# Optimization experiments

Measured on AMD Instinct MI355X. Metric: run time of the kernel, lower is better.

## Reference

```python
import jax, jax.numpy as jnp
import numpy as np

B, D, P, C = 4096, 512, 256, 8
LAMBDA = 1.0


def setup_inputs() -> dict:
    key = jax.random.key(0)
    k1, k2, k3, k4 = jax.random.split(key, 4)
    x = jax.random.normal(k1, (B, D), dtype=jnp.float32)
    y = jax.random.randint(k2, (B,), 0, C, dtype=jnp.int32)
    prototypes = jax.random.normal(k3, (P, D), dtype=jnp.float32)
    # omega initialized as eye + 0.01*randn per class, like the torch module
    omega = jnp.eye(D, dtype=jnp.float32)[None] + 0.01 * jax.random.normal(k4, (C, D, D), dtype=jnp.float32)
    prototype_labels = (jnp.arange(P, dtype=jnp.int32) % C).astype(jnp.int32)
    return {"x": x, "y": y, "prototypes": prototypes, "omega": omega, "prototype_labels": prototype_labels}


def reference(x, y, prototypes, omega, prototype_labels):
    # transformed inputs per class: tx[c,b,:] = omega[c] @ x[b]
    tx = jnp.einsum('cij,bj->cbi', omega, x)                     # [C,B,D]
    # transformed prototypes under every class omega, then pick each
    # prototype's own class matrix: tp[p,:] = omega[label[p]] @ w[p]
    tp_all = jnp.einsum('cij,pj->cpi', omega, prototypes)        # [C,P,D]
    tp = tp_all[prototype_labels, jnp.arange(P)]                 # [P,D]
    # squared distances via expansion ||a-b||^2 = |a|^2 + |b|^2 - 2ab
    dots = jnp.einsum('cbd,pd->cbp', tx, tp)                     # [C,B,P]
    x2 = jnp.sum(tx * tx, axis=-1)                               # [C,B]
    p2 = jnp.sum(tp * tp, axis=-1)                               # [P]
    dist_all = x2[:, :, None] + p2[None, None, :] - 2.0 * dots   # [C,B,P]
    # each prototype uses the omega of its own class
    dist = dist_all[prototype_labels, :, jnp.arange(P)].T        # [B,P]
    same = prototype_labels[None, :] == y[:, None]               # [B,P]
    inf = jnp.float32(jnp.inf)
    pos = jnp.min(jnp.where(same, dist, inf), axis=1)            # [B]
    neg = jnp.min(jnp.where(same, inf, dist), axis=1)            # [B]
    mu = (pos - neg) / (pos + neg)
    loss = jnp.mean(jax.nn.sigmoid(LAMBDA * mu))
    loss = loss + 0.01 * jnp.linalg.norm(omega.reshape(-1))
    return loss
```

## Files before the change

### kernel.cpp

```cpp
#include <hip/hip_runtime.h>
#include <math.h>

typedef unsigned short ushort_t;
typedef __attribute__((ext_vector_type(8))) short short8;
typedef __attribute__((ext_vector_type(4))) float f32x4;

#define B_N 4096
#define D_N 512
#define P_N 256
#define C_N 8

#define ACC_OFF   0
#define P2G_OFF   256
#define X2_OFF    1280
#define XB_OFF    132352
#define OMB_OFF   (XB_OFF + B_N*D_N*2)
#define TPG_OFF   (OMB_OFF + C_N*D_N*D_N*2)
#define UG_OFF    (TPG_OFF + P_N*D_N*2)
#define OMBT_OFF  (UG_OFF + P_N*D_N*2)
#define MINB_OFF  OMBT_OFF

#define MFMA16(a, b, c) __builtin_amdgcn_mfma_f32_16x16x32_bf16(a, b, c, 0, 0, 0)

__device__ inline ushort_t f2bf(float f) {
    union { float f; unsigned u; } v; v.f = f;
    unsigned r = v.u + 0x7FFFu + ((v.u >> 16) & 1u);
    return (ushort_t)(r >> 16);
}

__device__ __forceinline__ void gll16(const ushort_t* g, ushort_t* l) {
    __builtin_amdgcn_global_load_lds((const __attribute__((address_space(1))) void*)g,
                                     (__attribute__((address_space(3))) void*)l, 16, 0, 0);
}

__global__ void k_cast(const float* __restrict__ x, const float* __restrict__ omega,
                       ushort_t* __restrict__ xb, ushort_t* __restrict__ omb,
                       ushort_t* __restrict__ ombT, float* __restrict__ oss) {
    __shared__ ushort_t T[64][72];
    __shared__ float red[4];
    int t = threadIdx.x;
    if (blockIdx.x < 1024) {
        int idx = blockIdx.x * 256 + t;
        const float4* x4 = (const float4*)x;
        float4 a = x4[idx * 2], b = x4[idx * 2 + 1];
        union { ushort_t s[8]; uint4 v; } o;
        o.s[0] = f2bf(a.x); o.s[1] = f2bf(a.y); o.s[2] = f2bf(a.z); o.s[3] = f2bf(a.w);
        o.s[4] = f2bf(b.x); o.s[5] = f2bf(b.y); o.s[6] = f2bf(b.z); o.s[7] = f2bf(b.w);
        ((uint4*)xb)[idx] = o.v;
        return;
    }
    int bid = blockIdx.x - 1024;
    int c = bid >> 6, by = (bid >> 3) & 7, bx = bid & 7;
    int r0 = by * 64, c0 = bx * 64;
    int r = t >> 2, seg = t & 3;
    const float* src = omega + ((size_t)c * D_N + r0 + r) * D_N + c0 + seg * 16;
    float4 v0 = ((const float4*)src)[0], v1 = ((const float4*)src)[1];
    float4 v2 = ((const float4*)src)[2], v3 = ((const float4*)src)[3];
    float s = v0.x*v0.x + v0.y*v0.y + v0.z*v0.z + v0.w*v0.w
            + v1.x*v1.x + v1.y*v1.y + v1.z*v1.z + v1.w*v1.w
            + v2.x*v2.x + v2.y*v2.y + v2.z*v2.z + v2.w*v2.w
            + v3.x*v3.x + v3.y*v3.y + v3.z*v3.z + v3.w*v3.w;
    union { ushort_t s[16]; uint4 v[2]; } o;
    float vv[16] = {v0.x,v0.y,v0.z,v0.w, v1.x,v1.y,v1.z,v1.w,
                    v2.x,v2.y,v2.z,v2.w, v3.x,v3.y,v3.z,v3.w};
    #pragma unroll
    for (int j = 0; j < 16; ++j) o.s[j] = f2bf(vv[j]);
    uint4* dst = (uint4*)(omb + ((size_t)c * D_N + r0 + r) * D_N + c0 + seg * 16);
    dst[0] = o.v[0]; dst[1] = o.v[1];
    #pragma unroll
    for (int j = 0; j < 16; ++j) T[seg * 16 + j][r] = o.s[j];
    __syncthreads();
    int jr = t >> 2, sg2 = t & 3;
    uint4 w0 = *(uint4*)&T[jr][sg2 * 16];
    uint4 w1 = *(uint4*)&T[jr][sg2 * 16 + 8];
    uint4* dstT = (uint4*)(ombT + ((size_t)c * D_N + c0 + jr) * D_N + r0 + sg2 * 16);
    dstT[0] = w0; dstT[1] = w1;
    #pragma unroll
    for (int off = 32; off > 0; off >>= 1) s += __shfl_down(s, off);
    if ((t & 63) == 0) red[t >> 6] = s;
    __syncthreads();
    if (t == 0) atomicAdd(oss, red[0] + red[1] + red[2] + red[3]);
}

__global__ __launch_bounds__(256) void k_tp(const float* __restrict__ prot,
                                            const ushort_t* __restrict__ omb,
                                            ushort_t* __restrict__ tpg,
                                            float* __restrict__ p2g) {
    int i0 = blockIdx.x * 64, c = blockIdx.y;
    __shared__ ushort_t As[32][72];
    __shared__ ushort_t Bs[64][72];
    int t = threadIdx.x, w = t >> 6, lane = t & 63;
    int g = lane >> 4, cl = lane & 15;
    f32x4 acc[2] = {{0,0,0,0},{0,0,0,0}};
    for (int k0 = 0; k0 < D_N; k0 += 64) {
        __syncthreads();
        {
            int m = t >> 3, seg = t & 7;
            const float* ap = prot + ((size_t)(c + 8 * m)) * D_N + k0 + seg * 8;
            float4 u0 = ((const float4*)ap)[0], u1 = ((const float4*)ap)[1];
            union { ushort_t s[8]; uint4 v; } o;
            o.s[0]=f2bf(u0.x); o.s[1]=f2bf(u0.y); o.s[2]=f2bf(u0.z); o.s[3]=f2bf(u0.w);
            o.s[4]=f2bf(u1.x); o.s[5]=f2bf(u1.y); o.s[6]=f2bf(u1.z); o.s[7]=f2bf(u1.w);
            *(uint4*)&As[m][seg * 8] = o.v;
        }
        {
            int r = t >> 2, sg = t & 3;
            const uint4* bp = (const uint4*)(omb + ((size_t)c * D_N + i0 + r) * D_N + k0 + sg * 16);
            *(uint4*)&Bs[r][sg * 16] = bp[0];
            *(uint4*)&Bs[r][sg * 16 + 8] = bp[1];
        }
        __syncthreads();
        #pragma unroll
        for (int kk = 0; kk < 2; ++kk) {
            int koff = kk * 32 + g * 8;
            short8 bfr = *(const short8*)&Bs[w * 16 + cl][koff];
            #pragma unroll
            for (int mt = 0; mt < 2; ++mt) {
                short8 afr = *(const short8*)&As[mt * 16 + cl][koff];
                acc[mt] = MFMA16(afr, bfr, acc[mt]);
            }
        }
    }
    #pragma unroll
    for (int mt = 0; mt < 2; ++mt)
        #pragma unroll
        for (int reg = 0; reg < 4; ++reg) {
            float v = acc[mt][reg];
            int m = mt * 16 + g * 4 + reg;
            int i = i0 + w * 16 + cl;
            tpg[((size_t)c * 32 + m) * D_N + i] = f2bf(v);
            float s = v * v;
            s += __shfl_xor(s, 1); s += __shfl_xor(s, 2);
            s += __shfl_xor(s, 4); s += __shfl_xor(s, 8);
            if (cl == 0) atomicAdd(&p2g[c * 32 + m], s);
        }
}

__global__ __launch_bounds__(256) void k_u(const ushort_t* __restrict__ tpg,
                                           const ushort_t* __restrict__ ombT,
                                           ushort_t* __restrict__ ug) {
    int j0 = blockIdx.x * 64, c = blockIdx.y;
    __shared__ ushort_t As[32][72];
    __shared__ ushort_t Bs[64][72];
    int t = threadIdx.x, w = t >> 6, lane = t & 63;
    int g = lane >> 4, cl = lane & 15;
    f32x4 acc[2] = {{0,0,0,0},{0,0,0,0}};
    for (int k0 = 0; k0 < D_N; k0 += 64) {
        __syncthreads();
        {
            int m = t >> 3, seg = t & 7;
            *(uint4*)&As[m][seg * 8] =
                *(const uint4*)(tpg + ((size_t)c * 32 + m) * D_N + k0 + seg * 8);
        }
        {
            int r = t >> 2, sg = t & 3;
            const uint4* bp = (const uint4*)(ombT + ((size_t)c * D_N + j0 + r) * D_N + k0 + sg * 16);
            *(uint4*)&Bs[r][sg * 16] = bp[0];
            *(uint4*)&Bs[r][sg * 16 + 8] = bp[1];
        }
        __syncthreads();
        #pragma unroll
        for (int kk = 0; kk < 2; ++kk) {
            int koff = kk * 32 + g * 8;
            short8 bfr = *(const short8*)&Bs[w * 16 + cl][koff];
            #pragma unroll
            for (int mt = 0; mt < 2; ++mt) {
                short8 afr = *(const short8*)&As[mt * 16 + cl][koff];
                acc[mt] = MFMA16(afr, bfr, acc[mt]);
            }
        }
    }
    #pragma unroll
    for (int mt = 0; mt < 2; ++mt)
        #pragma unroll
        for (int reg = 0; reg < 4; ++reg) {
            int m = mt * 16 + g * 4 + reg;
            int j = j0 + w * 16 + cl;
            ug[((size_t)c * 32 + m) * D_N + j] = f2bf(acc[mt][reg]);
        }
}

__global__ __launch_bounds__(256, 2) void k_x2d(const ushort_t* __restrict__ xb,
                                                const ushort_t* __restrict__ omb,
                                                const ushort_t* __restrict__ ug,
                                                const float* __restrict__ p2g,
                                                float* __restrict__ x2,
                                                float* __restrict__ minb) {
    int c  = blockIdx.y;
    int b0 = blockIdx.z * 128;
    int t = threadIdx.x, w = t >> 6, lane = t & 63;
    int g = lane >> 4, cl = lane & 15;
    int srow = lane >> 2, spos = lane & 3;
    int ch = ((g - (cl >> 1)) & 3) * 8;

    __shared__ ushort_t Xs[2][128][32];
    __shared__ ushort_t Os[2][256][32];
    __shared__ float red[128][2];

    if (blockIdx.x < 2) {
        int i0 = blockIdx.x * 256;
        int qr = w >> 1, qc = w & 1;
        f32x4 acc[4][8];
        #pragma unroll
        for (int mt = 0; mt < 4; ++mt)
            #pragma unroll
            for (int nt = 0; nt < 8; ++nt) acc[mt][nt] = (f32x4){0,0,0,0};
        #pragma unroll
        for (int i = 0; i < 2; ++i) {
            int rb = w * 32 + i * 16;
            int r  = rb + srow;
            int cg = (spos + (r >> 1)) & 3;
            gll16(xb + (size_t)(b0 + r) * D_N + cg * 8, &Xs[0][rb][0]);
        }
        #pragma unroll
        for (int i = 0; i < 4; ++i) {
            int rb = w * 64 + i * 16;
            int r  = rb + srow;
            int cg = (spos + (r >> 1)) & 3;
            gll16(omb + ((size_t)c * D_N + i0 + r) * D_N + cg * 8, &Os[0][rb][0]);
        }
        __syncthreads();
        for (int s = 0; s < 16; ++s) {
            int cb = s & 1, nb = cb ^ 1;
            if (s < 15) {
                int k1 = (s + 1) * 32;
                #pragma unroll
                for (int i = 0; i < 2; ++i) {
                    int rb = w * 32 + i * 16;
                    int r  = rb + srow;
                    int cg = (spos + (r >> 1)) & 3;
                    gll16(xb + (size_t)(b0 + r) * D_N + k1 + cg * 8, &Xs[nb][rb][0]);
                }
                #pragma unroll
                for (int i = 0; i < 4; ++i) {
                    int rb = w * 64 + i * 16;
                    int r  = rb + srow;
                    int cg = (spos + (r >> 1)) & 3;
                    gll16(omb + ((size_t)c * D_N + i0 + r) * D_N + k1 + cg * 8, &Os[nb][rb][0]);
                }
            }
            short8 a[4], b[8];
            #pragma unroll
            for (int mt = 0; mt < 4; ++mt)
                a[mt] = *(const short8*)&Xs[cb][qr * 64 + mt * 16 + cl][ch];
            #pragma unroll
            for (int nt = 0; nt < 8; ++nt)
                b[nt] = *(const short8*)&Os[cb][qc * 128 + nt * 16 + cl][ch];
            #pragma unroll
            for (int mt = 0; mt < 4; ++mt)
                #pragma unroll
                for (int nt = 0; nt < 8; ++nt)
                    acc[mt][nt] = MFMA16(a[mt], b[nt], acc[mt][nt]);
            __syncthreads();
        }
        #pragma unroll
        for (int mt = 0; mt < 4; ++mt)
            #pragma unroll
            for (int reg = 0; reg < 4; ++reg) {
                float s = 0.f;
                #pragma unroll
                for (int nt = 0; nt < 8; ++nt) s += acc[mt][nt][reg] * acc[mt][nt][reg];
                s += __shfl_xor(s, 1); s += __shfl_xor(s, 2);
                s += __shfl_xor(s, 4); s += __shfl_xor(s, 8);
                if (cl == 0) red[qr * 64 + mt * 16 + g * 4 + reg][qc] = s;
            }
        __syncthreads();
        if (t < 128) atomicAdd(&x2[(size_t)(b0 + t) * C_N + c], red[t][0] + red[t][1]);
    } else {
        f32x4 acc[2][2];
        #pragma unroll
        for (int mt = 0; mt < 2; ++mt)
            #pragma unroll
            for (int nt = 0; nt < 2; ++nt) acc[mt][nt] = (f32x4){0,0,0,0};
        #pragma unroll
        for (int i = 0; i < 2; ++i) {
            int rb = w * 32 + i * 16;
            int r  = rb + srow;
            int cg = (spos + (r >> 1)) & 3;
            gll16(xb + (size_t)(b0 + r) * D_N + cg * 8, &Xs[0][rb][0]);
        }
        if (w < 2) {
            int rb = w * 16;
            int r  = rb + srow;
            int cg = (spos + (r >> 1)) & 3;
            gll16(ug + ((size_t)c * 32 + r) * D_N + cg * 8, &Os[0][rb][0]);
        }
        __syncthreads();
        for (int s = 0; s < 16; ++s) {
            int cb = s & 1, nb = cb ^ 1;
            if (s < 15) {
                int k1 = (s + 1) * 32;
                #pragma unroll
                for (int i = 0; i < 2; ++i) {
                    int rb = w * 32 + i * 16;
                    int r  = rb + srow;
                    int cg = (spos + (r >> 1)) & 3;
                    gll16(xb + (size_t)(b0 + r) * D_N + k1 + cg * 8, &Xs[nb][rb][0]);
                }
                if (w < 2) {
                    int rb = w * 16;
                    int r  = rb + srow;
                    int cg = (spos + (r >> 1)) & 3;
                    gll16(ug + ((size_t)c * 32 + r) * D_N + k1 + cg * 8, &Os[nb][rb][0]);
                }
            }
            short8 a[2], b[2];
            #pragma unroll
            for (int mt = 0; mt < 2; ++mt)
                a[mt] = *(const short8*)&Xs[cb][w * 32 + mt * 16 + cl][ch];
            #pragma unroll
            for (int nt = 0; nt < 2; ++nt)
                b[nt] = *(const short8*)&Os[cb][nt * 16 + cl][ch];
            #pragma unroll
            for (int mt = 0; mt < 2; ++mt)
                #pragma unroll
                for (int nt = 0; nt < 2; ++nt)
                    acc[mt][nt] = MFMA16(a[mt], b[nt], acc[mt][nt]);
            __syncthreads();
        }
        #pragma unroll
        for (int mt = 0; mt < 2; ++mt)
            #pragma unroll
            for (int reg = 0; reg < 4; ++reg) {
                float v = INFINITY;
                #pragma unroll
                for (int nt = 0; nt < 2; ++nt) {
                    int q = c * 32 + nt * 16 + cl;
                    v = fminf(v, p2g[q] - 2.f * acc[mt][nt][reg]);
                }
                v = fminf(v, __shfl_xor(v, 1)); v = fminf(v, __shfl_xor(v, 2));
                v = fminf(v, __shfl_xor(v, 4)); v = fminf(v, __shfl_xor(v, 8));
                if (cl == 0)
                    minb[(size_t)(b0 + w * 32 + mt * 16 + g * 4 + reg) * C_N + c] = v;
            }
    }
}

__global__ void k_mu(const float* __restrict__ x2, const float* __restrict__ minb,
                     const int* __restrict__ y, float* __restrict__ accs,
                     float* __restrict__ out) {
    int t = threadIdx.x;
    int b = blockIdx.x * 256 + t;
    int yb = y[b];
    float d[8];
    #pragma unroll
    for (int cc = 0; cc < 8; ++cc)
        d[cc] = x2[(size_t)b * C_N + cc] + minb[(size_t)b * C_N + cc];
    float pos = d[yb];
    float neg = INFINITY;
    #pragma unroll
    for (int cc = 0; cc < 8; ++cc)
        if (cc != yb) neg = fminf(neg, d[cc]);
    float mu = (pos - neg) / (pos + neg);
    float s = 1.f / (1.f + expf(-mu));
    #pragma unroll
    for (int off = 32; off > 0; off >>= 1) s += __shfl_down(s, off);
    __shared__ float red[4];
    if ((t & 63) == 0) red[t >> 6] = s;
    __syncthreads();
    if (t == 0) {
        atomicAdd(accs, red[0] + red[1] + red[2] + red[3]);
        __threadfence();
        unsigned n = atomicAdd((unsigned int*)(accs + 2), 1u);
        if (n == (unsigned)(B_N / 256 - 1)) {
            float ls  = atomicAdd(accs, 0.f);
            float oss = atomicAdd(accs + 1, 0.f);
            out[0] = ls * (1.f / (float)B_N) + 0.01f * sqrtf(oss);
        }
    }
}

extern "C" void kernel_launch(void* const* d_in, const int* in_sizes, int n_in,
                              void* d_out, int out_size, void* d_ws, size_t ws_size,
                              hipStream_t stream) {
    (void)in_sizes; (void)n_in; (void)out_size; (void)ws_size;
    const float* x     = (const float*)d_in[0];
    const int*   y     = (const int*)d_in[1];
    const float* prot  = (const float*)d_in[2];
    const float* omega = (const float*)d_in[3];

    char* ws = (char*)d_ws;
    float*    accs = (float*)(ws + ACC_OFF);
    float*    p2g  = (float*)(ws + P2G_OFF);
    float*    x2   = (float*)(ws + X2_OFF);
    ushort_t* xb   = (ushort_t*)(ws + XB_OFF);
    ushort_t* omb  = (ushort_t*)(ws + OMB_OFF);
    ushort_t* tpg  = (ushort_t*)(ws + TPG_OFF);
    ushort_t* ug   = (ushort_t*)(ws + UG_OFF);
    ushort_t* ombT = (ushort_t*)(ws + OMBT_OFF);
    float*    minb = (float*)(ws + MINB_OFF);

    (void)hipMemsetAsync(ws, 0, XB_OFF, stream);
    k_cast   <<<1536, 256, 0, stream>>>(x, omega, xb, omb, ombT, accs + 1);
    k_tp     <<<dim3(8, C_N), 256, 0, stream>>>(prot, omb, tpg, p2g);
    k_u      <<<dim3(8, C_N), 256, 0, stream>>>(tpg, ombT, ug);
    k_x2d    <<<dim3(3, C_N, B_N / 128), 256, 0, stream>>>(xb, omb, ug, p2g, x2, minb);
    k_mu     <<<B_N / 256, 256, 0, stream>>>(x2, minb, y, accs, (float*)d_out);
}
```

Before: 137.7 us.

## Fuse prototype chain into x2 kernel and merge dot-min with loss reduction

```diff
diff --git a/kernel.cpp b/kernel.cpp
--- a/kernel.cpp
+++ b/kernel.cpp
@@ -15,10 +15,8 @@
 #define X2_OFF    1280
 #define XB_OFF    132352
 #define OMB_OFF   (XB_OFF + B_N*D_N*2)
-#define TPG_OFF   (OMB_OFF + C_N*D_N*D_N*2)
-#define UG_OFF    (TPG_OFF + P_N*D_N*2)
+#define UG_OFF    (OMB_OFF + C_N*D_N*D_N*2)
 #define OMBT_OFF  (UG_OFF + P_N*D_N*2)
-#define MINB_OFF  OMBT_OFF
 
 #define MFMA16(a, b, c) __builtin_amdgcn_mfma_f32_16x16x32_bf16(a, b, c, 0, 0, 0)
 
@@ -82,290 +80,272 @@
     if (t == 0) atomicAdd(oss, red[0] + red[1] + red[2] + red[3]);
 }
 
-__global__ __launch_bounds__(256) void k_tp(const float* __restrict__ prot,
-                                            const ushort_t* __restrict__ omb,
-                                            ushort_t* __restrict__ tpg,
-                                            float* __restrict__ p2g) {
-    int i0 = blockIdx.x * 64, c = blockIdx.y;
-    __shared__ ushort_t As[32][72];
-    __shared__ ushort_t Bs[64][72];
+__global__ __launch_bounds__(256, 2) void k_big(const float* __restrict__ prot,
+                                                const ushort_t* __restrict__ xb,
+                                                const ushort_t* __restrict__ omb,
+                                                const ushort_t* __restrict__ ombT,
+                                                ushort_t* __restrict__ ug,
+                                                float* __restrict__ p2g,
+                                                float* __restrict__ x2) {
+    __shared__ union {
+        struct { ushort_t Xs[2][128][32]; ushort_t Os[2][256][32]; float red[128][2]; } x;
+        struct { ushort_t As[32][72]; ushort_t Bs[64][72]; ushort_t tp[32][520]; float p2p[4][32]; } p;
+    } S;
+    int bid = blockIdx.x;
     int t = threadIdx.x, w = t >> 6, lane = t & 63;
     int g = lane >> 4, cl = lane & 15;
-    f32x4 acc[2] = {{0,0,0,0},{0,0,0,0}};
-    for (int k0 = 0; k0 < D_N; k0 += 64) {
+
+    if (bid < 8) {
+        int c = bid;
+        float p2r[2][4];
+        #pragma unroll
+        for (int mt = 0; mt < 2; ++mt)
+            #pragma unroll
+            for (int reg = 0; reg < 4; ++reg) p2r[mt][reg] = 0.f;
+        for (int i0 = 0; i0 < D_N; i0 += 64) {
+            f32x4 acc[2] = {{0,0,0,0},{0,0,0,0}};
+            for (int k0 = 0; k0 < D_N; k0 += 64) {
+                __syncthreads();
+                {
+                    int m = t >> 3, seg = t & 7;
+                    const float* ap = prot + ((size_t)(c + 8 * m)) * D_N + k0 + seg * 8;
+                    float4 u0 = ((const float4*)ap)[0], u1 = ((const float4*)ap)[1];
+                    union { ushort_t s[8]; uint4 v; } o;
+                    o.s[0]=f2bf(u0.x); o.s[1]=f2bf(u0.y); o.s[2]=f2bf(u0.z); o.s[3]=f2bf(u0.w);
+                    o.s[4]=f2bf(u1.x); o.s[5]=f2bf(u1.y); o.s[6]=f2bf(u1.z); o.s[7]=f2bf(u1.w);
+                    *(uint4*)&S.p.As[m][seg * 8] = o.v;
+                }
+                {
+                    int r = t >> 2, sg = t & 3;
+                    const uint4* bp = (const uint4*)(omb + ((size_t)c * D_N + i0 + r) * D_N + k0 + sg * 16);
+                    *(uint4*)&S.p.Bs[r][sg * 16] = bp[0];
+                    *(uint4*)&S.p.Bs[r][sg * 16 + 8] = bp[1];
+                }
+                __syncthreads();
+                #pragma unroll
+                for (int kk = 0; kk < 2; ++kk) {
+                    int koff = kk * 32 + g * 8;
+                    short8 bfr = *(const short8*)&S.p.Bs[w * 16 + cl][koff];
+                    #pragma unroll
+                    for (int mt = 0; mt < 2; ++mt) {
+                        short8 afr = *(const short8*)&S.p.As[mt * 16 + cl][koff];
+                        acc[mt] = MFMA16(afr, bfr, acc[mt]);
+                    }
+                }
+            }
+            #pragma unroll
+            for (int mt = 0; mt < 2; ++mt)
+                #pragma unroll
+                for (int reg = 0; reg < 4; ++reg) {
+                    float v = acc[mt][reg];
+                    int m = mt * 16 + g * 4 + reg;
+                    S.p.tp[m][i0 + w * 16 + cl] = f2bf(v);
+                    p2r[mt][reg] += v * v;
+                }
+        }
+        #pragma unroll
+        for (int mt = 0; mt < 2; ++mt)
+            #pragma unroll
+            for (int reg = 0; reg < 4; ++reg) {
+                float s = p2r[mt][reg];
+                s += __shfl_xor(s, 1); s += __shfl_xor(s, 2);
+                s += __shfl_xor(s, 4); s += __shfl_xor(s, 8);
+                if (cl == 0) S.p.p2p[w][mt * 16 + g * 4 + reg] = s;
+            }
         __syncthreads();
-        {
-            int m = t >> 3, seg = t & 7;
-            const float* ap = prot + ((size_t)(c + 8 * m)) * D_N + k0 + seg * 8;
-            float4 u0 = ((const float4*)ap)[0], u1 = ((const float4*)ap)[1];
-            union { ushort_t s[8]; uint4 v; } o;
-            o.s[0]=f2bf(u0.x); o.s[1]=f2bf(u0.y); o.s[2]=f2bf(u0.z); o.s[3]=f2bf(u0.w);
-            o.s[4]=f2bf(u1.x); o.s[5]=f2bf(u1.y); o.s[6]=f2bf(u1.z); o.s[7]=f2bf(u1.w);
-            *(uint4*)&As[m][seg * 8] = o.v;
-        }
-        {
-            int r = t >> 2, sg = t & 3;
-            const uint4* bp = (const uint4*)(omb + ((size_t)c * D_N + i0 + r) * D_N + k0 + sg * 16);
-            *(uint4*)&Bs[r][sg * 16] = bp[0];
-            *(uint4*)&Bs[r][sg * 16 + 8] = bp[1];
-        }
+        if (t < 32) p2g[c * 32 + t] = S.p.p2p[0][t] + S.p.p2p[1][t] + S.p.p2p[2][t] + S.p.p2p[3][t];
+        for (int j0 = 0; j0 < D_N; j0 += 64) {
+            f32x4 acc[2] = {{0,0,0,0},{0,0,0,0}};
+            for (int k0 = 0; k0 < D_N; k0 += 64) {
+                __syncthreads();
+                {
+                    int r = t >> 2, sg = t & 3;
+                    const uint4* bp = (const uint4*)(ombT + ((size_t)c * D_N + j0 + r) * D_N + k0 + sg * 16);
+                    *(uint4*)&S.p.Bs[r][sg * 16] = bp[0];
+                    *(uint4*)&S.p.Bs[r][sg * 16 + 8] = bp[1];
+                }
+                __syncthreads();
+                #pragma unroll
+                for (int kk = 0; kk < 2; ++kk) {
+                    int koff = kk * 32 + g * 8;
+                    short8 bfr = *(const short8*)&S.p.Bs[w * 16 + cl][koff];
+                    #pragma unroll
+                    for (int mt = 0; mt < 2; ++mt) {
+                        short8 afr = *(const short8*)&S.p.tp[mt * 16 + cl][k0 + koff];
+                        acc[mt] = MFMA16(afr, bfr, acc[mt]);
+                    }
+                }
+            }
+            #pragma unroll
+            for (int mt = 0; mt < 2; ++mt)
+                #pragma unroll
+                for (int reg = 0; reg < 4; ++reg) {
+                    int m = mt * 16 + g * 4 + reg;
+                    int j = j0 + w * 16 + cl;
+                    ug[((size_t)c * 32 + m) * D_N + j] = f2bf(acc[mt][reg]);
+                }
+        }
+        return;
+    }
+
+    int idx = bid - 8;
+    int ic = idx & 1, c = (idx >> 1) & 7;
+    int b0 = (idx >> 4) * 128;
+    int i0 = ic * 256;
+    int srow = lane >> 2, spos = lane & 3;
+    int ch = ((g - (cl >> 1)) & 3) * 8;
+    int qr = w >> 1, qc = w & 1;
+    f32x4 acc[4][8];
+    #pragma unroll
+    for (int mt = 0; mt < 4; ++mt)
+        #pragma unroll
+        for (int nt = 0; nt < 8; ++nt) acc[mt][nt] = (f32x4){0,0,0,0};
+    #pragma unroll
+    for (int i = 0; i < 2; ++i) {
+        int rb = w * 32 + i * 16;
+        int r  = rb + srow;
+        int cg = (spos + (r >> 1)) & 3;
+        gll16(xb + (size_t)(b0 + r) * D_N + cg * 8, &S.x.Xs[0][rb][0]);
+    }
+    #pragma unroll
+    for (int i = 0; i < 4; ++i) {
+        int rb = w * 64 + i * 16;
+        int r  = rb + srow;
+        int cg = (spos + (r >> 1)) & 3;
+        gll16(omb + ((size_t)c * D_N + i0 + r) * D_N + cg * 8, &S.x.Os[0][rb][0]);
+    }
+    __syncthreads();
+    for (int s = 0; s < 16; ++s) {
+        int cb = s & 1, nb = cb ^ 1;
+        if (s < 15) {
+            int k1 = (s + 1) * 32;
+            #pragma unroll
+            for (int i = 0; i < 2; ++i) {
+                int rb = w * 32 + i * 16;
+                int r  = rb + srow;
+                int cg = (spos + (r >> 1)) & 3;
+                gll16(xb + (size_t)(b0 + r) * D_N + k1 + cg * 8, &S.x.Xs[nb][rb][0]);
+            }
+            #pragma unroll
+            for (int i = 0; i < 4; ++i) {
+                int rb = w * 64 + i * 16;
+                int r  = rb + srow;
+                int cg = (spos + (r >> 1)) & 3;
+                gll16(omb + ((size_t)c * D_N + i0 + r) * D_N + k1 + cg * 8, &S.x.Os[nb][rb][0]);
+            }
+        }
+        short8 a[4], b[8];
+        #pragma unroll
+        for (int mt = 0; mt < 4; ++mt)
+            a[mt] = *(const short8*)&S.x.Xs[cb][qr * 64 + mt * 16 + cl][ch];
+        #pragma unroll
+        for (int nt = 0; nt < 8; ++nt)
+            b[nt] = *(const short8*)&S.x.Os[cb][qc * 128 + nt * 16 + cl][ch];
+        #pragma unroll
+        for (int mt = 0; mt < 4; ++mt)
+            #pragma unroll
+            for (int nt = 0; nt < 8; ++nt)
+                acc[mt][nt] = MFMA16(a[mt], b[nt], acc[mt][nt]);
         __syncthreads();
-        #pragma unroll
-        for (int kk = 0; kk < 2; ++kk) {
-            int koff = kk * 32 + g * 8;
-            short8 bfr = *(const short8*)&Bs[w * 16 + cl][koff];
-            #pragma unroll
-            for (int mt = 0; mt < 2; ++mt) {
-                short8 afr = *(const short8*)&As[mt * 16 + cl][koff];
-                acc[mt] = MFMA16(afr, bfr, acc[mt]);
-            }
-        }
-    }
-    #pragma unroll
-    for (int mt = 0; mt < 2; ++mt)
+    }
+    #pragma unroll
+    for (int mt = 0; mt < 4; ++mt)
         #pragma unroll
         for (int reg = 0; reg < 4; ++reg) {
-            float v = acc[mt][reg];
-            int m = mt * 16 + g * 4 + reg;
-            int i = i0 + w * 16 + cl;
-            tpg[((size_t)c * 32 + m) * D_N + i] = f2bf(v);
-            float s = v * v;
+            float s = 0.f;
+            #pragma unroll
+            for (int nt = 0; nt < 8; ++nt) s += acc[mt][nt][reg] * acc[mt][nt][reg];
             s += __shfl_xor(s, 1); s += __shfl_xor(s, 2);
             s += __shfl_xor(s, 4); s += __shfl_xor(s, 8);
-            if (cl == 0) atomicAdd(&p2g[c * 32 + m], s);
-        }
-}
-
-__global__ __launch_bounds__(256) void k_u(const ushort_t* __restrict__ tpg,
-                                           const ushort_t* __restrict__ ombT,
-                                           ushort_t* __restrict__ ug) {
-    int j0 = blockIdx.x * 64, c = blockIdx.y;
-    __shared__ ushort_t As[32][72];
-    __shared__ ushort_t Bs[64][72];
-    int t = threadIdx.x, w = t >> 6, lane = t & 63;
-    int g = lane >> 4, cl = lane & 15;
-    f32x4 acc[2] = {{0,0,0,0},{0,0,0,0}};
-    for (int k0 = 0; k0 < D_N; k0 += 64) {
-        __syncthreads();
-        {
-            int m = t >> 3, seg = t & 7;
-            *(uint4*)&As[m][seg * 8] =
-                *(const uint4*)(tpg + ((size_t)c * 32 + m) * D_N + k0 + seg * 8);
-        }
-        {
-            int r = t >> 2, sg = t & 3;
-            const uint4* bp = (const uint4*)(ombT + ((size_t)c * D_N + j0 + r) * D_N + k0 + sg * 16);
-            *(uint4*)&Bs[r][sg * 16] = bp[0];
-            *(uint4*)&Bs[r][sg * 16 + 8] = bp[1];
-        }
-        __syncthreads();
-        #pragma unroll
-        for (int kk = 0; kk < 2; ++kk) {
-            int koff = kk * 32 + g * 8;
-            short8 bfr = *(const short8*)&Bs[w * 16 + cl][koff];
-            #pragma unroll
-            for (int mt = 0; mt < 2; ++mt) {
-                short8 afr = *(const short8*)&As[mt * 16 + cl][koff];
-                acc[mt] = MFMA16(afr, bfr, acc[mt]);
-            }
-        }
-    }
-    #pragma unroll
-    for (int mt = 0; mt < 2; ++mt)
-        #pragma unroll
-        for (int reg = 0; reg < 4; ++reg) {
-            int m = mt * 16 + g * 4 + reg;
-            int j = j0 + w * 16 + cl;
-            ug[((size_t)c * 32 + m) * D_N + j] = f2bf(acc[mt][reg]);
-        }
-}
-
-__global__ __launch_bounds__(256, 2) void k_x2d(const ushort_t* __restrict__ xb,
-                                                const ushort_t* __restrict__ omb,
-                                                const ushort_t* __restrict__ ug,
-                                                const float* __restrict__ p2g,
-                                                float* __restrict__ x2,
-                                                float* __restrict__ minb) {
-    int c  = blockIdx.y;
-    int b0 = blockIdx.z * 128;
+            if (cl == 0) S.x.red[qr * 64 + mt * 16 + g * 4 + reg][qc] = s;
+        }
+    __syncthreads();
+    if (t < 128) atomicAdd(&x2[(size_t)(b0 + t) * C_N + c], S.x.red[t][0] + S.x.red[t][1]);
+}
+
+__global__ __launch_bounds__(256) void k_dm(const ushort_t* __restrict__ xb,
+                                            const ushort_t* __restrict__ ug,
+                                            const float* __restrict__ p2g,
+                                            const float* __restrict__ x2,
+                                            const int* __restrict__ y,
+                                            float* __restrict__ accs,
+                                            float* __restrict__ out) {
+    int b0 = blockIdx.x * 64;
     int t = threadIdx.x, w = t >> 6, lane = t & 63;
     int g = lane >> 4, cl = lane & 15;
     int srow = lane >> 2, spos = lane & 3;
     int ch = ((g - (cl >> 1)) & 3) * 8;
-
-    __shared__ ushort_t Xs[2][128][32];
-    __shared__ ushort_t Os[2][256][32];
-    __shared__ float red[128][2];
-
-    if (blockIdx.x < 2) {
-        int i0 = blockIdx.x * 256;
-        int qr = w >> 1, qc = w & 1;
-        f32x4 acc[4][8];
-        #pragma unroll
-        for (int mt = 0; mt < 4; ++mt)
-            #pragma unroll
-            for (int nt = 0; nt < 8; ++nt) acc[mt][nt] = (f32x4){0,0,0,0};
-        #pragma unroll
-        for (int i = 0; i < 2; ++i) {
-            int rb = w * 32 + i * 16;
-            int r  = rb + srow;
-            int cg = (spos + (r >> 1)) & 3;
-            gll16(xb + (size_t)(b0 + r) * D_N + cg * 8, &Xs[0][rb][0]);
-        }
-        #pragma unroll
-        for (int i = 0; i < 4; ++i) {
-            int rb = w * 64 + i * 16;
-            int r  = rb + srow;
-            int cg = (spos + (r >> 1)) & 3;
-            gll16(omb + ((size_t)c * D_N + i0 + r) * D_N + cg * 8, &Os[0][rb][0]);
-        }
+    int cg0 = (spos + (srow >> 1)) & 3;
+    __shared__ ushort_t Xs[2][64][32];
+    __shared__ ushort_t Us[2][256][32];
+    __shared__ float minb[64][8];
+    f32x4 acc[2][8];
+    #pragma unroll
+    for (int nt = 0; nt < 2; ++nt)
+        #pragma unroll
+        for (int cc = 0; cc < 8; ++cc) acc[nt][cc] = (f32x4){0,0,0,0};
+    gll16(xb + (size_t)(b0 + w * 16 + srow) * D_N + cg0 * 8, &Xs[0][w * 16][0]);
+    #pragma unroll
+    for (int i = 0; i < 4; ++i) {
+        int q = w * 64 + i * 16;
+        gll16(ug + (size_t)(q + srow) * D_N + cg0 * 8, &Us[0][q][0]);
+    }
+    __syncthreads();
+    for (int sl = 0; sl < 16; ++sl) {
+        int cb = sl & 1, nb = cb ^ 1;
+        if (sl < 15) {
+            int k1 = (sl + 1) * 32;
+            gll16(xb + (size_t)(b0 + w * 16 + srow) * D_N + k1 + cg0 * 8, &Xs[nb][w * 16][0]);
+            #pragma unroll
+            for (int i = 0; i < 4; ++i) {
+                int q = w * 64 + i * 16;
+                gll16(ug + (size_t)(q + srow) * D_N + k1 + cg0 * 8, &Us[nb][q][0]);
+            }
+        }
+        short8 a = *(const short8*)&Xs[cb][w * 16 + cl][ch];
+        #pragma unroll
+        for (int cc = 0; cc < 8; ++cc)
+            #pragma unroll
+            for (int nt = 0; nt < 2; ++nt) {
+                short8 bf = *(const short8*)&Us[cb][cc * 32 + nt * 16 + cl][ch];
+                acc[nt][cc] = MFMA16(a, bf, acc[nt][cc]);
+            }
         __syncthreads();
-        for (int s = 0; s < 16; ++s) {
-            int cb = s & 1, nb = cb ^ 1;
-            if (s < 15) {
-                int k1 = (s + 1) * 32;
-                #pragma unroll
-                for (int i = 0; i < 2; ++i) {
-                    int rb = w * 32 + i * 16;
-                    int r  = rb + srow;
-                    int cg = (spos + (r >> 1)) & 3;
-                    gll16(xb + (size_t)(b0 + r) * D_N + k1 + cg * 8, &Xs[nb][rb][0]);
-                }
-                #pragma unroll
-                for (int i = 0; i < 4; ++i) {
-                    int rb = w * 64 + i * 16;
-                    int r  = rb + srow;
-                    int cg = (spos + (r >> 1)) & 3;
-                    gll16(omb + ((size_t)c * D_N + i0 + r) * D_N + k1 + cg * 8, &Os[nb][rb][0]);
-                }
-            }
-            short8 a[4], b[8];
-            #pragma unroll
-            for (int mt = 0; mt < 4; ++mt)
-                a[mt] = *(const short8*)&Xs[cb][qr * 64 + mt * 16 + cl][ch];
-            #pragma unroll
-            for (int nt = 0; nt < 8; ++nt)
-                b[nt] = *(const short8*)&Os[cb][qc * 128 + nt * 16 + cl][ch];
-            #pragma unroll
-            for (int mt = 0; mt < 4; ++mt)
-                #pragma unroll
-                for (int nt = 0; nt < 8; ++nt)
-                    acc[mt][nt] = MFMA16(a[mt], b[nt], acc[mt][nt]);
-            __syncthreads();
-        }
-        #pragma unroll
-        for (int mt = 0; mt < 4; ++mt)
-            #pragma unroll
-            for (int reg = 0; reg < 4; ++reg) {
-                float s = 0.f;
-                #pragma unroll
-                for (int nt = 0; nt < 8; ++nt) s += acc[mt][nt][reg] * acc[mt][nt][reg];
-                s += __shfl_xor(s, 1); s += __shfl_xor(s, 2);
-                s += __shfl_xor(s, 4); s += __shfl_xor(s, 8);
-                if (cl == 0) red[qr * 64 + mt * 16 + g * 4 + reg][qc] = s;
-            }
-        __syncthreads();
-        if (t < 128) atomicAdd(&x2[(size_t)(b0 + t) * C_N + c], red[t][0] + red[t][1]);
-    } else {
-        f32x4 acc[2][2];
-        #pragma unroll
-        for (int mt = 0; mt < 2; ++mt)
-            #pragma unroll
-            for (int nt = 0; nt < 2; ++nt) acc[mt][nt] = (f32x4){0,0,0,0};
-        #pragma unroll
-        for (int i = 0; i < 2; ++i) {
-            int rb = w * 32 + i * 16;
-            int r  = rb + srow;
-            int cg = (spos + (r >> 1)) & 3;
-            gll16(xb + (size_t)(b0 + r) * D_N + cg * 8, &Xs[0][rb][0]);
-        }
-        if (w < 2) {
-            int rb = w * 16;
-            int r  = rb + srow;
-            int cg = (spos + (r >> 1)) & 3;
-            gll16(ug + ((size_t)c * 32 + r) * D_N + cg * 8, &Os[0][rb][0]);
-        }
-        __syncthreads();
-        for (int s = 0; s < 16; ++s) {
-            int cb = s & 1, nb = cb ^ 1;
-            if (s < 15) {
-                int k1 = (s + 1) * 32;
-                #pragma unroll
-                for (int i = 0; i < 2; ++i) {
-                    int rb = w * 32 + i * 16;
-                    int r  = rb + srow;
-                    int cg = (spos + (r >> 1)) & 3;
-                    gll16(xb + (size_t)(b0 + r) * D_N + k1 + cg * 8, &Xs[nb][rb][0]);
-                }
-                if (w < 2) {
-                    int rb = w * 16;
-                    int r  = rb + srow;
-                    int cg = (spos + (r >> 1)) & 3;
-                    gll16(ug + ((size_t)c * 32 + r) * D_N + k1 + cg * 8, &Os[nb][rb][0]);
-                }
-            }
-            short8 a[2], b[2];
-            #pragma unroll
-            for (int mt = 0; mt < 2; ++mt)
-                a[mt] = *(const short8*)&Xs[cb][w * 32 + mt * 16 + cl][ch];
+    }
+    #pragma unroll
+    for (int cc = 0; cc < 8; ++cc)
+        #pragma unroll
+        for (int reg = 0; reg < 4; ++reg) {
+            float v = INFINITY;
             #pragma unroll
             for (int nt = 0; nt < 2; ++nt)
-                b[nt] = *(const short8*)&Os[cb][nt * 16 + cl][ch];
-            #pragma unroll
-            for (int mt = 0; mt < 2; ++mt)
-                #pragma unroll
-                for (int nt = 0; nt < 2; ++nt)
-                    acc[mt][nt] = MFMA16(a[mt], b[nt], acc[mt][nt]);
-            __syncthreads();
-        }
-        #pragma unroll
-        for (int mt = 0; mt < 2; ++mt)
-            #pragma unroll
-            for (int reg = 0; reg < 4; ++reg) {
-                float v = INFINITY;
-                #pragma unroll
-                for (int nt = 0; nt < 2; ++nt) {
-                    int q = c * 32 + nt * 16 + cl;
-                    v = fminf(v, p2g[q] - 2.f * acc[mt][nt][reg]);
-                }
-                v = fminf(v, __shfl_xor(v, 1)); v = fminf(v, __shfl_xor(v, 2));
-                v = fminf(v, __shfl_xor(v, 4)); v = fminf(v, __shfl_xor(v, 8));
-                if (cl == 0)
-                    minb[(size_t)(b0 + w * 32 + mt * 16 + g * 4 + reg) * C_N + c] = v;
-            }
-    }
-}
-
-__global__ void k_mu(const float* __restrict__ x2, const float* __restrict__ minb,
-                     const int* __restrict__ y, float* __restrict__ accs,
-                     float* __restrict__ out) {
-    int t = threadIdx.x;
-    int b = blockIdx.x * 256 + t;
-    int yb = y[b];
-    float d[8];
-    #pragma unroll
-    for (int cc = 0; cc < 8; ++cc)
-        d[cc] = x2[(size_t)b * C_N + cc] + minb[(size_t)b * C_N + cc];
-    float pos = d[yb];
-    float neg = INFINITY;
-    #pragma unroll
-    for (int cc = 0; cc < 8; ++cc)
-        if (cc != yb) neg = fminf(neg, d[cc]);
-    float mu = (pos - neg) / (pos + neg);
-    float s = 1.f / (1.f + expf(-mu));
-    #pragma unroll
-    for (int off = 32; off > 0; off >>= 1) s += __shfl_down(s, off);
-    __shared__ float red[4];
-    if ((t & 63) == 0) red[t >> 6] = s;
-    __syncthreads();
-    if (t == 0) {
-        atomicAdd(accs, red[0] + red[1] + red[2] + red[3]);
-        __threadfence();
-        unsigned n = atomicAdd((unsigned int*)(accs + 2), 1u);
-        if (n == (unsigned)(B_N / 256 - 1)) {
-            float ls  = atomicAdd(accs, 0.f);
-            float oss = atomicAdd(accs + 1, 0.f);
-            out[0] = ls * (1.f / (float)B_N) + 0.01f * sqrtf(oss);
+                v = fminf(v, p2g[cc * 32 + nt * 16 + cl] - 2.f * acc[nt][cc][reg]);
+            v = fminf(v, __shfl_xor(v, 1)); v = fminf(v, __shfl_xor(v, 2));
+            v = fminf(v, __shfl_xor(v, 4)); v = fminf(v, __shfl_xor(v, 8));
+            if (cl == 0) minb[w * 16 + g * 4 + reg][cc] = v;
+        }
+    __syncthreads();
+    if (t < 64) {
+        int b = b0 + t, yb = y[b];
+        float pos = 0.f, neg = INFINITY;
+        #pragma unroll
+        for (int cc = 0; cc < 8; ++cc) {
+            float d = x2[(size_t)b * C_N + cc] + minb[t][cc];
+            if (cc == yb) pos = d; else neg = fminf(neg, d);
+        }
+        float mu = (pos - neg) / (pos + neg);
+        float s = 1.f / (1.f + expf(-mu));
+        #pragma unroll
+        for (int off = 32; off > 0; off >>= 1) s += __shfl_down(s, off);
+        if (t == 0) {
+            atomicAdd(accs, s);
+            __threadfence();
+            unsigned n = atomicAdd((unsigned*)(accs + 2), 1u);
+            if (n == 63u) {
+                float ls  = atomicAdd(accs, 0.f);
+                float oss = atomicAdd(accs + 1, 0.f);
+                out[0] = ls * (1.f / (float)B_N) + 0.01f * sqrtf(oss);
+            }
         }
     }
 }
@@ -385,15 +365,11 @@
     float*    x2   = (float*)(ws + X2_OFF);
     ushort_t* xb   = (ushort_t*)(ws + XB_OFF);
     ushort_t* omb  = (ushort_t*)(ws + OMB_OFF);
-    ushort_t* tpg  = (ushort_t*)(ws + TPG_OFF);
     ushort_t* ug   = (ushort_t*)(ws + UG_OFF);
     ushort_t* ombT = (ushort_t*)(ws + OMBT_OFF);
-    float*    minb = (float*)(ws + MINB_OFF);
 
     (void)hipMemsetAsync(ws, 0, XB_OFF, stream);
-    k_cast   <<<1536, 256, 0, stream>>>(x, omega, xb, omb, ombT, accs + 1);
-    k_tp     <<<dim3(8, C_N), 256, 0, stream>>>(prot, omb, tpg, p2g);
-    k_u      <<<dim3(8, C_N), 256, 0, stream>>>(tpg, ombT, ug);
-    k_x2d    <<<dim3(3, C_N, B_N / 128), 256, 0, stream>>>(xb, omb, ug, p2g, x2, minb);
-    k_mu     <<<B_N / 256, 256, 0, stream>>>(x2, minb, y, accs, (float*)d_out);
-}
+    k_cast <<<1536, 256, 0, stream>>>(x, omega, xb, omb, ombT, accs + 1);
+    k_big  <<<520, 256, 0, stream>>>(prot, xb, omb, ombT, ug, p2g, x2);
+    k_dm   <<<64, 256, 0, stream>>>(xb, ug, p2g, x2, y, accs, (float*)d_out);
+}
```

After: 208.7 us. 51.5% more time.
